# Performance work log

Hardware: AMD Instinct MI355X
Metric: run time of the kernel (lower is better)

Reference implementation:

```python
import jax, jax.numpy as jnp
import numpy as np

E, R, K, D, B = 100000, 1000, 200, 256, 65536  # entities, relations, bundle heads, emb dim, batch


def setup_inputs() -> dict:
    key = jax.random.key(0)
    ks = jax.random.split(key, 12)
    ent_emb = jax.random.normal(ks[0], (E, D), dtype=jnp.float32)
    ent_emb = ent_emb / jnp.linalg.norm(ent_emb, axis=1, keepdims=True)  # xavier + L2 row-normalize
    heads = jax.random.normal(ks[1], (K, D), dtype=jnp.float32)
    heads = heads / jnp.linalg.norm(heads, axis=1, keepdims=True)  # normalize_vvrel_embeddings
    bases = jax.random.normal(ks[2], (R, 2, D), dtype=jnp.float32)
    bases = bases / jnp.linalg.norm(bases, axis=2, keepdims=True)  # normalize_all_rows
    rel2head = jax.random.randint(ks[3], (R,), 0, K)              # r_id2_vrr[rel][0] -> head idx
    rel2mult = jnp.where(jax.random.bernoulli(ks[4], 0.5, (R,)), 1.0, -1.0).astype(jnp.float32)  # r_id2_vrr[rel][1]
    return {
        'pos_h': jax.random.randint(ks[5], (B,), 0, E),
        'pos_t': jax.random.randint(ks[6], (B,), 0, E),
        'pos_r': jax.random.randint(ks[7], (B,), 0, R),
        'neg_h': jax.random.randint(ks[8], (B,), 0, E),
        'neg_t': jax.random.randint(ks[9], (B,), 0, E),
        'neg_r': jax.random.randint(ks[10], (B,), 0, R),
        'ent_emb': ent_emb, 'heads': heads, 'bases': bases,
        'rel2head': rel2head, 'rel2mult': rel2mult,
    }


def _transint_scores(pos_h, pos_t, pos_r, neg_h, neg_t, ent_emb, heads, bases, rel2head, rel2mult):
    # vvrel_embedding_func: head embedding scaled by +-1 multiplier
    r_e = heads[rel2head[pos_r]] * rel2mult[pos_r][:, None]           # [B, D]
    pos_sub = ent_emb[pos_h] + r_e - ent_emb[pos_t]                    # [B, D]
    neg_sub = ent_emb[neg_h] + r_e - ent_emb[neg_t]                    # [B, D] (note: uses pos_r_e, as in source)
    sub = jnp.concatenate([pos_sub, neg_sub], axis=0)                  # [2B, D]
    A = bases[jnp.concatenate([pos_r, pos_r], axis=0)]                 # [2B, 2, D] per-sample basis (comb_mats gather)
    # ATA and closed-form 2x2 inverse (module's `inverse`)
    ATA = jnp.einsum('bkd,bld->bkl', A, A)                             # [2B, 2, 2]
    a, b = ATA[:, 0, 0], ATA[:, 0, 1]
    c, d = ATA[:, 1, 0], ATA[:, 1, 1]
    det = a * d - b * c
    safe_det = jnp.where(det != 0, det, 1.0)
    inv_reg = jnp.stack([jnp.stack([d, -b], -1), jnp.stack([-c, a], -1)], -2) / safe_det[:, None, None]
    inv_fb = jnp.eye(2, dtype=ATA.dtype)[None] / a[:, None, None]      # fallback when det == 0
    ATA_inv = jnp.where((det != 0)[:, None, None], inv_reg, inv_fb)    # [2B, 2, 2]
    # P @ sub with P = I - A^T (A A^T)^{-1} A, applied without materializing P
    Asub = jnp.einsum('bkd,bd->bk', A, sub)                            # [2B, 2]
    proj = sub - jnp.einsum('bkd,bk->bd', A, jnp.einsum('bkl,bl->bk', ATA_inv, Asub))
    score = jnp.sum(proj ** 2, axis=1)                                 # L1_flag = False -> squared L2
    nb = pos_h.shape[0]
    return score[:nb], score[nb:]


def reference(pos_h, pos_t, pos_r, neg_h, neg_t, neg_r, ent_emb, heads, bases, rel2head, rel2mult):
    return _transint_scores(pos_h, pos_t, pos_r, neg_h, neg_t, ent_emb, heads, bases, rel2head, rel2mult)
```

## Files before the change

### kernel.cpp

```cpp
#include <hip/hip_runtime.h>

#define D 256
#define D4 (D/4)

__device__ inline float dot4(const float4 u, const float4 v) {
    return u.x*v.x + u.y*v.y + u.z*v.z + u.w*v.w;
}

__device__ inline float wsum(float v) {
    #pragma unroll
    for (int off = 32; off > 0; off >>= 1)
        v += __shfl_xor(v, off, 64);
    return v;
}

__global__ __launch_bounds__(256) void transint_kernel(
    const int*   __restrict__ pos_h,
    const int*   __restrict__ pos_t,
    const int*   __restrict__ pos_r,
    const int*   __restrict__ neg_h,
    const int*   __restrict__ neg_t,
    const float* __restrict__ ent_emb,
    const float* __restrict__ heads,
    const float* __restrict__ bases,
    const int*   __restrict__ rel2head,
    const float* __restrict__ rel2mult,
    float*       __restrict__ out,
    int nB)
{
    const int wave = (blockIdx.x * blockDim.x + threadIdx.x) >> 6;
    const int lane = threadIdx.x & 63;
    if (wave >= nB) return;
    const int b = wave;

    const int r  = pos_r[b];
    const int ph = pos_h[b];
    const int pt = pos_t[b];
    const int nh = neg_h[b];
    const int nt = neg_t[b];
    const int hd = rel2head[r];
    const float mult = rel2mult[r];

    const float4* e    = (const float4*)ent_emb;
    const float4* hrow = (const float4*)(heads + (size_t)hd * D);
    const float4* arow = (const float4*)(bases + (size_t)r * 2 * D);

    float4 a0 = arow[lane];
    float4 a1 = arow[D4 + lane];
    float4 re = hrow[lane];
    re.x *= mult; re.y *= mult; re.z *= mult; re.w *= mult;

    float4 eph = e[(size_t)ph * D4 + lane];
    float4 ept = e[(size_t)pt * D4 + lane];
    float4 enh = e[(size_t)nh * D4 + lane];
    float4 ent = e[(size_t)nt * D4 + lane];

    float4 ps, ns;
    ps.x = eph.x + re.x - ept.x;  ns.x = enh.x + re.x - ent.x;
    ps.y = eph.y + re.y - ept.y;  ns.y = enh.y + re.y - ent.y;
    ps.z = eph.z + re.z - ept.z;  ns.z = enh.z + re.z - ent.z;
    ps.w = eph.w + re.w - ept.w;  ns.w = enh.w + re.w - ent.w;

    float aa = wsum(dot4(a0, a0));
    float ab = wsum(dot4(a0, a1));
    float dd = wsum(dot4(a1, a1));
    float p0 = wsum(dot4(a0, ps));
    float p1 = wsum(dot4(a1, ps));
    float n0 = wsum(dot4(a0, ns));
    float n1 = wsum(dot4(a1, ns));

    float det = aa * dd - ab * ab;
    float cp0, cp1, cn0, cn1;
    if (det != 0.0f) {
        float inv = 1.0f / det;
        cp0 = (dd * p0 - ab * p1) * inv;
        cp1 = (aa * p1 - ab * p0) * inv;
        cn0 = (dd * n0 - ab * n1) * inv;
        cn1 = (aa * n1 - ab * n0) * inv;
    } else {
        float inv = 1.0f / aa;
        cp0 = p0 * inv; cp1 = p1 * inv;
        cn0 = n0 * inv; cn1 = n1 * inv;
    }

    float4 pp, pn;
    pp.x = ps.x - cp0 * a0.x - cp1 * a1.x;  pn.x = ns.x - cn0 * a0.x - cn1 * a1.x;
    pp.y = ps.y - cp0 * a0.y - cp1 * a1.y;  pn.y = ns.y - cn0 * a0.y - cn1 * a1.y;
    pp.z = ps.z - cp0 * a0.z - cp1 * a1.z;  pn.z = ns.z - cn0 * a0.z - cn1 * a1.z;
    pp.w = ps.w - cp0 * a0.w - cp1 * a1.w;  pn.w = ns.w - cn0 * a0.w - cn1 * a1.w;

    float sp = wsum(dot4(pp, pp));
    float sn = wsum(dot4(pn, pn));

    if (lane == 0) {
        out[b]      = sp;
        out[nB + b] = sn;
    }
}

extern "C" void kernel_launch(void* const* d_in, const int* in_sizes, int n_in,
                              void* d_out, int out_size, void* d_ws, size_t ws_size,
                              hipStream_t stream) {
    const int*   pos_h    = (const int*)  d_in[0];
    const int*   pos_t    = (const int*)  d_in[1];
    const int*   pos_r    = (const int*)  d_in[2];
    const int*   neg_h    = (const int*)  d_in[3];
    const int*   neg_t    = (const int*)  d_in[4];
    const float* ent_emb  = (const float*)d_in[6];
    const float* heads    = (const float*)d_in[7];
    const float* bases    = (const float*)d_in[8];
    const int*   rel2head = (const int*)  d_in[9];
    const float* rel2mult = (const float*)d_in[10];
    float* out = (float*)d_out;

    const int nB = in_sizes[0];
    const int waves_per_block = 4;
    dim3 grid((nB + waves_per_block - 1) / waves_per_block);
    dim3 block(256);
    transint_kernel<<<grid, block, 0, stream>>>(
        pos_h, pos_t, pos_r, neg_h, neg_t,
        ent_emb, heads, bases, rel2head, rel2mult,
        out, nB);
}
```

Baseline: 190.8 us.

## Precompute per-relation inverse Gram and rel vectors; 16 lanes per sample with algebraic norm

Adds a pre-kernel that computes, once per relation, the scaled head vector and the 2x2 inverse Gram matrix along with the Gram entries, and stores them in workspace. The main kernel now handles four samples per wave with 16 lanes each. It computes the squared norm of the projection in closed form from ||s||², A·s and the Gram entries, which removes the second pass and one set of reductions. The trade-offs are a second launch, workspace traffic, and possible loss of precision from cancellation in the expanded norm formula.

```diff
diff --git a/kernel.cpp b/kernel.cpp
--- a/kernel.cpp
+++ b/kernel.cpp
@@ -14,34 +14,22 @@
     return v;
 }
 
-__global__ __launch_bounds__(256) void transint_kernel(
-    const int*   __restrict__ pos_h,
-    const int*   __restrict__ pos_t,
-    const int*   __restrict__ pos_r,
-    const int*   __restrict__ neg_h,
-    const int*   __restrict__ neg_t,
-    const float* __restrict__ ent_emb,
+__global__ __launch_bounds__(256) void transint_pre(
     const float* __restrict__ heads,
     const float* __restrict__ bases,
     const int*   __restrict__ rel2head,
     const float* __restrict__ rel2mult,
-    float*       __restrict__ out,
-    int nB)
+    float*       __restrict__ re_buf,
+    float*       __restrict__ par_buf,
+    int R)
 {
     const int wave = (blockIdx.x * blockDim.x + threadIdx.x) >> 6;
     const int lane = threadIdx.x & 63;
-    if (wave >= nB) return;
-    const int b = wave;
+    if (wave >= R) return;
+    const int r = wave;
 
-    const int r  = pos_r[b];
-    const int ph = pos_h[b];
-    const int pt = pos_t[b];
-    const int nh = neg_h[b];
-    const int nt = neg_t[b];
     const int hd = rel2head[r];
     const float mult = rel2mult[r];
-
-    const float4* e    = (const float4*)ent_emb;
     const float4* hrow = (const float4*)(heads + (size_t)hd * D);
     const float4* arow = (const float4*)(bases + (size_t)r * 2 * D);
 
@@ -49,50 +37,116 @@
     float4 a1 = arow[D4 + lane];
     float4 re = hrow[lane];
     re.x *= mult; re.y *= mult; re.z *= mult; re.w *= mult;
-
-    float4 eph = e[(size_t)ph * D4 + lane];
-    float4 ept = e[(size_t)pt * D4 + lane];
-    float4 enh = e[(size_t)nh * D4 + lane];
-    float4 ent = e[(size_t)nt * D4 + lane];
-
-    float4 ps, ns;
-    ps.x = eph.x + re.x - ept.x;  ns.x = enh.x + re.x - ent.x;
-    ps.y = eph.y + re.y - ept.y;  ns.y = enh.y + re.y - ent.y;
-    ps.z = eph.z + re.z - ept.z;  ns.z = enh.z + re.z - ent.z;
-    ps.w = eph.w + re.w - ept.w;  ns.w = enh.w + re.w - ent.w;
+    ((float4*)(re_buf + (size_t)r * D))[lane] = re;
 
     float aa = wsum(dot4(a0, a0));
     float ab = wsum(dot4(a0, a1));
     float dd = wsum(dot4(a1, a1));
-    float p0 = wsum(dot4(a0, ps));
-    float p1 = wsum(dot4(a1, ps));
-    float n0 = wsum(dot4(a0, ns));
-    float n1 = wsum(dot4(a1, ns));
 
     float det = aa * dd - ab * ab;
-    float cp0, cp1, cn0, cn1;
+    float m00, m01, m11;
     if (det != 0.0f) {
         float inv = 1.0f / det;
-        cp0 = (dd * p0 - ab * p1) * inv;
-        cp1 = (aa * p1 - ab * p0) * inv;
-        cn0 = (dd * n0 - ab * n1) * inv;
-        cn1 = (aa * n1 - ab * n0) * inv;
+        m00 = dd * inv; m01 = -ab * inv; m11 = aa * inv;
     } else {
         float inv = 1.0f / aa;
-        cp0 = p0 * inv; cp1 = p1 * inv;
-        cn0 = n0 * inv; cn1 = n1 * inv;
+        m00 = inv; m01 = 0.0f; m11 = inv;
+    }
+    if (lane == 0) {
+        float* p = par_buf + (size_t)r * 8;
+        p[0] = m00; p[1] = m01; p[2] = m11;
+        p[3] = aa;  p[4] = ab;  p[5] = dd;
+        p[6] = 0.0f; p[7] = 0.0f;
+    }
+}
+
+__global__ __launch_bounds__(256) void transint_main(
+    const int*   __restrict__ pos_h,
+    const int*   __restrict__ pos_t,
+    const int*   __restrict__ pos_r,
+    const int*   __restrict__ neg_h,
+    const int*   __restrict__ neg_t,
+    const float* __restrict__ ent_emb,
+    const float* __restrict__ bases,
+    const float* __restrict__ re_buf,
+    const float* __restrict__ par_buf,
+    float*       __restrict__ out,
+    int nB)
+{
+    const int wave = (blockIdx.x * blockDim.x + threadIdx.x) >> 6;
+    const int lane = threadIdx.x & 63;
+    const int g    = lane >> 4;
+    const int gl   = lane & 15;
+    const int b    = wave * 4 + g;
+    if (b >= nB) return;
+
+    const int r  = pos_r[b];
+    const int ph = pos_h[b];
+    const int pt = pos_t[b];
+    const int nh = neg_h[b];
+    const int nt = neg_t[b];
+
+    const float4* e   = (const float4*)ent_emb;
+    const float4* a0p = (const float4*)(bases + (size_t)r * 2 * D);
+    const float4* a1p = a0p + D4;
+    const float4* rep = (const float4*)(re_buf + (size_t)r * D);
+    const float4* php = e + (size_t)ph * D4;
+    const float4* ptp = e + (size_t)pt * D4;
+    const float4* nhp = e + (size_t)nh * D4;
+    const float4* ntp = e + (size_t)nt * D4;
+
+    float p0 = 0.f, p1 = 0.f, n0 = 0.f, n1 = 0.f, ssp = 0.f, ssn = 0.f;
+
+    #pragma unroll
+    for (int c = 0; c < 4; ++c) {
+        const int idx = gl + 16 * c;
+        float4 a0 = a0p[idx];
+        float4 a1 = a1p[idx];
+        float4 re = rep[idx];
+        float4 eh = php[idx];
+        float4 et = ptp[idx];
+        float4 xh = nhp[idx];
+        float4 xt = ntp[idx];
+
+        float4 ps, ns;
+        ps.x = eh.x + re.x - et.x;  ns.x = xh.x + re.x - xt.x;
+        ps.y = eh.y + re.y - et.y;  ns.y = xh.y + re.y - xt.y;
+        ps.z = eh.z + re.z - et.z;  ns.z = xh.z + re.z - xt.z;
+        ps.w = eh.w + re.w - et.w;  ns.w = xh.w + re.w - xt.w;
+
+        p0  += dot4(a0, ps);
+        p1  += dot4(a1, ps);
+        n0  += dot4(a0, ns);
+        n1  += dot4(a1, ns);
+        ssp += dot4(ps, ps);
+        ssn += dot4(ns, ns);
     }
 
-    float4 pp, pn;
-    pp.x = ps.x - cp0 * a0.x - cp1 * a1.x;  pn.x = ns.x - cn0 * a0.x - cn1 * a1.x;
-    pp.y = ps.y - cp0 * a0.y - cp1 * a1.y;  pn.y = ns.y - cn0 * a0.y - cn1 * a1.y;
-    pp.z = ps.z - cp0 * a0.z - cp1 * a1.z;  pn.z = ns.z - cn0 * a0.z - cn1 * a1.z;
-    pp.w = ps.w - cp0 * a0.w - cp1 * a1.w;  pn.w = ns.w - cn0 * a0.w - cn1 * a1.w;
+    #pragma unroll
+    for (int off = 8; off > 0; off >>= 1) {
+        p0  += __shfl_xor(p0,  off, 64);
+        p1  += __shfl_xor(p1,  off, 64);
+        n0  += __shfl_xor(n0,  off, 64);
+        n1  += __shfl_xor(n1,  off, 64);
+        ssp += __shfl_xor(ssp, off, 64);
+        ssn += __shfl_xor(ssn, off, 64);
+    }
 
-    float sp = wsum(dot4(pp, pp));
-    float sn = wsum(dot4(pn, pn));
+    const float* par = par_buf + (size_t)r * 8;
+    const float m00 = par[0], m01 = par[1], m11 = par[2];
+    const float aa  = par[3], ab  = par[4], dd  = par[5];
 
-    if (lane == 0) {
+    float c0 = m00 * p0 + m01 * p1;
+    float c1 = m01 * p0 + m11 * p1;
+    float sp = ssp - 2.f * (p0 * c0 + p1 * c1)
+             + (aa * c0 * c0 + 2.f * ab * c0 * c1 + dd * c1 * c1);
+
+    float d0 = m00 * n0 + m01 * n1;
+    float d1 = m01 * n0 + m11 * n1;
+    float sn = ssn - 2.f * (n0 * d0 + n1 * d1)
+             + (aa * d0 * d0 + 2.f * ab * d0 * d1 + dd * d1 * d1);
+
+    if (gl == 0) {
         out[b]      = sp;
         out[nB + b] = sn;
     }
@@ -114,11 +168,23 @@
     float* out = (float*)d_out;
 
     const int nB = in_sizes[0];
-    const int waves_per_block = 4;
-    dim3 grid((nB + waves_per_block - 1) / waves_per_block);
-    dim3 block(256);
-    transint_kernel<<<grid, block, 0, stream>>>(
-        pos_h, pos_t, pos_r, neg_h, neg_t,
-        ent_emb, heads, bases, rel2head, rel2mult,
-        out, nB);
+    const int R  = in_sizes[9];
+
+    float* re_buf  = (float*)d_ws;
+    float* par_buf = re_buf + (size_t)R * D;
+
+    {
+        const int waves_per_block = 4;
+        dim3 grid((R + waves_per_block - 1) / waves_per_block);
+        transint_pre<<<grid, dim3(256), 0, stream>>>(
+            heads, bases, rel2head, rel2mult, re_buf, par_buf, R);
+    }
+
+    {
+        const int samples_per_block = 16;
+        dim3 grid((nB + samples_per_block - 1) / samples_per_block);
+        transint_main<<<grid, dim3(256), 0, stream>>>(
+            pos_h, pos_t, pos_r, neg_h, neg_t,
+            ent_emb, bases, re_buf, par_buf, out, nB);
+    }
 }
```

After: 195.2 us. 2.3% more time.
